# Kernel tuning notes

Measured on AMD Instinct MI355X. Metric: run time of the kernel, lower is better.

The kernel has to match this reference:

```python
import jax, jax.numpy as jnp
import numpy as np

N = 2048  # number of graph nodes


def setup_inputs() -> dict:
    key = jax.random.key(0)
    k1, k2, k3, k4 = jax.random.split(key, 4)
    # dense non-negative adjacency / association matrix
    A = jax.random.uniform(k1, (N, N), dtype=jnp.float32)
    # GTConv weights: layer0.conv1, layer0.conv2, layer1.conv1 (each (2,1,1,1))
    w1a = jax.random.normal(k2, (2, 1, 1, 1), dtype=jnp.float32)
    w1b = jax.random.normal(k3, (2, 1, 1, 1), dtype=jnp.float32)
    w2a = jax.random.normal(k4, (2, 1, 1, 1), dtype=jnp.float32)
    return {"A": A, "w1a": w1a, "w1b": w1b, "w2a": w2a}


def _gtconv(A4, w):
    # A4: (1,1,n,n); w: (2,1,1,1). softmax over dim=1 (singleton -> ones),
    # broadcast-multiply -> (2,1,n,n), sum over dim 0 -> (1,n,n)
    sw = jax.nn.softmax(w, axis=1)
    return jnp.sum(A4 * sw, axis=0)


def _norm(H):
    # H: (n,n). H <- diag(deg)^-1 @ (H + I), expressed as a row-scale
    # (identical math to the diagonal mm in the original).
    n = H.shape[0]
    H = H + jnp.eye(n, dtype=H.dtype)
    deg = jnp.sum(H, axis=1)
    deg = jnp.where(deg <= 1e-10, jnp.ones_like(deg), deg)
    return H / deg[:, None]


def reference(A, w1a, w1b, w2a):
    A4 = A[None, None]  # (1,1,n,n) after the forward's unsqueeze + broadcast
    # layer 0 (first=True)
    a = _gtconv(A4, w1a)            # (1,n,n)
    b = _gtconv(A4, w1b)            # (1,n,n)
    H = jnp.matmul(a, b)            # (1,n,n)
    # layer 1 (first=False): normalization of H[0], then bmm with conv(A)
    H_ = _norm(H[0])[None]          # (1,n,n)
    a2 = _gtconv(A4, w2a)           # (1,n,n)
    H2 = jnp.matmul(H_, a2)         # (1,n,n)
    return H2
```

## Files before the change

### kernel.cpp

```cpp
#include <hip/hip_runtime.h>
#include <stdint.h>

#define N 2048
#define TILE 128
#define BK 64
#define KH 16
#define RSTR 16
#define NN ((size_t)N * (size_t)N)

typedef unsigned short u16;
typedef __bf16 bf16x8 __attribute__((ext_vector_type(8)));
typedef unsigned short ushortx8 __attribute__((ext_vector_type(8)));
typedef float floatx4 __attribute__((ext_vector_type(4)));

static __device__ __forceinline__ u16 f2bf(float f) {
  unsigned int u = __builtin_bit_cast(unsigned int, f);
  return (u16)((u + 0x7fffu + ((u >> 16) & 1u)) >> 16);
}
static __device__ __forceinline__ float bf2f(u16 h) {
  unsigned int u = ((unsigned int)h) << 16;
  return __builtin_bit_cast(float, u);
}

static __device__ __forceinline__ void gload16(const u16* g, u16* l) {
  __builtin_amdgcn_global_load_lds(
      (const __attribute__((address_space(1))) void*)g,
      (__attribute__((address_space(3))) void*)l, 16, 0, 0);
}

__global__ void cast_tr(const float* __restrict__ A, u16* __restrict__ Ab,
                        u16* __restrict__ Abt) {
  __shared__ float tile[32][33];
  const int tx = threadIdx.x, ty = threadIdx.y;
  const int c = blockIdx.x * 32 + tx;
#pragma unroll
  for (int i = 0; i < 4; i++) {
    const int r = blockIdx.y * 32 + ty + i * 8;
    const float v = A[(size_t)r * N + c];
    Ab[(size_t)r * N + c] = f2bf(v);
    tile[ty + i * 8][tx] = v;
  }
  __syncthreads();
  const int r2 = blockIdx.y * 32 + tx;
#pragma unroll
  for (int i = 0; i < 4; i++) {
    const int c2 = blockIdx.x * 32 + ty + i * 8;
    Abt[(size_t)c2 * N + r2] = f2bf(tile[tx][ty + i * 8]);
  }
}

__device__ __forceinline__ void gemm_core(const u16* __restrict__ L,
                                          const u16* __restrict__ Rt,
                                          int row0, int col0,
                                          float res[4][4]) {
  __shared__ __align__(16) u16 As[2][2][TILE * BK];
  __shared__ __align__(16) u16 Bs[2][2][TILE * BK];

  const int t = threadIdx.x;
  const int lane = t & 63;
  const int w = t >> 6;
  const int h = w >> 3;
  const int wv = w & 7;

  const int rl = lane >> 3;
  const int cl = ((lane & 7) ^ rl) * 8;
  const int g0 = wv * 2;
  const u16* gA0 = L + (size_t)(row0 + g0 * 8 + rl) * N + h * (KH * BK) + cl;
  const u16* gA1 = gA0 + 8 * N;
  const u16* gB0 = Rt + (size_t)(col0 + g0 * 8 + rl) * N + h * (KH * BK) + cl;
  const u16* gB1 = gB0 + 8 * N;
  const int ld0 = g0 * 512;

  const int sub = wv;
  const int wr = (sub >> 2) * 64;
  const int wc = (sub & 3) * 32;
  const int lr = lane & 15;
  const int q = lane >> 4;
  const int lx = lr & 7;
  const int arow = (wr + lr) * BK;
  const int brow = (wc + lr) * BK;

  floatx4 acc[4][2];
#pragma unroll
  for (int i = 0; i < 4; i++)
#pragma unroll
    for (int j = 0; j < 2; j++) acc[i][j] = (floatx4){0.f, 0.f, 0.f, 0.f};

  gload16(gA0, &As[h][0][ld0]);
  gload16(gA1, &As[h][0][ld0 + 512]);
  gload16(gB0, &Bs[h][0][ld0]);
  gload16(gB1, &Bs[h][0][ld0 + 512]);
  __syncthreads();

#define GSTEP(i, cur, nxt)                                                    \
  {                                                                           \
    if ((i) + 1 < KH) {                                                       \
      gload16(gA0 + ((i) + 1) * BK, &As[h][nxt][ld0]);                        \
      gload16(gA1 + ((i) + 1) * BK, &As[h][nxt][ld0 + 512]);                  \
      gload16(gB0 + ((i) + 1) * BK, &Bs[h][nxt][ld0]);                        \
      gload16(gB1 + ((i) + 1) * BK, &Bs[h][nxt][ld0 + 512]);                  \
    }                                                                         \
    _Pragma("unroll") for (int kk = 0; kk < 2; kk++) {                        \
      bf16x8 af[4], bfr[2];                                                   \
      _Pragma("unroll") for (int mt = 0; mt < 4; mt++) af[mt] =               \
          __builtin_bit_cast(                                                 \
              bf16x8, *(const ushortx8*)&As[h][cur][arow + mt * 16 * BK +     \
                                                    ((kk * 4 + q) ^ lx) * 8]); \
      _Pragma("unroll") for (int nt = 0; nt < 2; nt++) bfr[nt] =              \
          __builtin_bit_cast(                                                 \
              bf16x8, *(const ushortx8*)&Bs[h][cur][brow + nt * 16 * BK +     \
                                                    ((kk * 4 + q) ^ lx) * 8]); \
      _Pragma("unroll") for (int mt = 0; mt < 4; mt++)                        \
          _Pragma("unroll") for (int nt = 0; nt < 2; nt++) acc[mt][nt] =      \
              __builtin_amdgcn_mfma_f32_16x16x32_bf16(af[mt], bfr[nt],        \
                                                      acc[mt][nt], 0, 0, 0);  \
    }                                                                         \
    __syncthreads();                                                          \
  }

  for (int io = 0; io < KH; io += 2) {
    GSTEP(io, 0, 1)
    GSTEP(io + 1, 1, 0)
  }
#undef GSTEP

  float* red = (float*)&As[0][0][0];
  const int oh = 1 - h;
  const int rship = (sub * 2 + oh) * (64 * RSTR);
  const int rkeep = (sub * 2 + h) * (64 * RSTR);
#pragma unroll
  for (int mt = 0; mt < 4; mt++)
#pragma unroll
    for (int r = 0; r < 4; r++) {
      const float vship = h ? acc[mt][0][r] : acc[mt][1][r];
      red[rship + (mt * 16 + q * 4 + r) * RSTR + lr] = vship;
    }
  __syncthreads();
#pragma unroll
  for (int mt = 0; mt < 4; mt++)
#pragma unroll
    for (int r = 0; r < 4; r++) {
      const float vkeep = h ? acc[mt][1][r] : acc[mt][0][r];
      res[mt][r] = vkeep + red[rkeep + (mt * 16 + q * 4 + r) * RSTR + lr];
    }
}

__global__ __launch_bounds__(1024, 4) void gemm_aa(const u16* __restrict__ Ab,
                                                   const u16* __restrict__ Abt,
                                                   u16* __restrict__ Mb) {
  const int row0 = blockIdx.y * TILE, col0 = blockIdx.x * TILE;
  float res[4][4];
  gemm_core(Ab, Abt, row0, col0, res);
  const int t = threadIdx.x;
  const int lane = t & 63, w = t >> 6;
  const int sub = w & 7, h = w >> 3;
  const int wr = (sub >> 2) * 64, wc = (sub & 3) * 32;
  const int lr = lane & 15, q = lane >> 4;
  const int cc = col0 + wc + h * 16 + lr;
#pragma unroll
  for (int mt = 0; mt < 4; mt++)
#pragma unroll
    for (int r = 0; r < 4; r++) {
      const int rr = row0 + wr + mt * 16 + q * 4 + r;
      Mb[(size_t)rr * N + cc] = f2bf(res[mt][r]);
    }
}

__global__ void rowsum_k(const u16* __restrict__ Mb, float* __restrict__ rdeg) {
  const int row = blockIdx.x;
  const int t = threadIdx.x;
  const ushortx8 v = *((const ushortx8*)(Mb + (size_t)row * N) + t);
  float s = 0.f;
#pragma unroll
  for (int j = 0; j < 8; j++) s += bf2f(v[j]);
#pragma unroll
  for (int off = 32; off > 0; off >>= 1) s += __shfl_down(s, off, 64);
  __shared__ float ws[4];
  if ((t & 63) == 0) ws[t >> 6] = s;
  __syncthreads();
  if (t == 0) {
    float d = 4.f * (ws[0] + ws[1] + ws[2] + ws[3]) + 1.f;
    if (d <= 1e-10f) d = 1.f;
    rdeg[row] = 1.f / d;
  }
}

__global__ __launch_bounds__(1024, 4) void gemm_ma(const u16* __restrict__ Mb,
                                                   const u16* __restrict__ Abt,
                                                   const float* __restrict__ A,
                                                   const float* __restrict__ rdeg,
                                                   float* __restrict__ out) {
  const int row0 = blockIdx.y * TILE, col0 = blockIdx.x * TILE;
  float res[4][4];
  gemm_core(Mb, Abt, row0, col0, res);
  const int t = threadIdx.x;
  const int lane = t & 63, w = t >> 6;
  const int sub = w & 7, h = w >> 3;
  const int wr = (sub >> 2) * 64, wc = (sub & 3) * 32;
  const int lr = lane & 15, q = lane >> 4;
  const int cc = col0 + wc + h * 16 + lr;
#pragma unroll
  for (int mt = 0; mt < 4; mt++)
#pragma unroll
    for (int r = 0; r < 4; r++) {
      const int rr = row0 + wr + mt * 16 + q * 4 + r;
      out[(size_t)rr * N + cc] =
          (8.f * res[mt][r] + 2.f * A[(size_t)rr * N + cc]) * rdeg[rr];
    }
}

extern "C" void kernel_launch(void* const* d_in, const int* in_sizes, int n_in,
                              void* d_out, int out_size, void* d_ws, size_t ws_size,
                              hipStream_t stream) {
  const float* A = (const float*)d_in[0];
  float* out = (float*)d_out;
  char* ws = (char*)d_ws;
  u16* Ab = (u16*)ws;
  u16* Abt = (u16*)(ws + NN * 2);
  u16* Mb = (u16*)(ws + NN * 4);
  float* rdeg = (float*)(ws + NN * 6);

  cast_tr<<<dim3(N / 32, N / 32), dim3(32, 8), 0, stream>>>(A, Ab, Abt);
  gemm_aa<<<dim3(N / TILE, N / TILE), 1024, 0, stream>>>(Ab, Abt, Mb);
  rowsum_k<<<N, 256, 0, stream>>>(Mb, rdeg);
  gemm_ma<<<dim3(N / TILE, N / TILE), 1024, 0, stream>>>(Mb, Abt, A, rdeg, out);
}
```

Baseline: 135.2 us.

## Restructure GEMM core into 4-way split-K with 64x64 warp tiles

Reorganizes the shared GEMM core so the 16 waves form four K-slices of four waves each. Each wave now computes a 64x64 sub-tile, up from 64x32, which raises MFMA work per LDS fragment load. The async global-to-LDS loads are replaced by register-staged loads written into padded LDS rows, with BK halved. A two-stage LDS reduction merges the four K partials and only half the waves write outputs. The cost is higher register pressure, extra reduction syncs, and software-pipelined register staging in place of direct LDS loads.

```diff
diff --git a/kernel.cpp b/kernel.cpp
--- a/kernel.cpp
+++ b/kernel.cpp
@@ -3,9 +3,10 @@
 
 #define N 2048
 #define TILE 128
-#define BK 64
-#define KH 16
-#define RSTR 16
+#define BK 32
+#define KQ 16
+#define LDSW 40
+#define XSTR 68
 #define NN ((size_t)N * (size_t)N)
 
 typedef unsigned short u16;
@@ -20,12 +21,6 @@
 static __device__ __forceinline__ float bf2f(u16 h) {
   unsigned int u = ((unsigned int)h) << 16;
   return __builtin_bit_cast(float, u);
-}
-
-static __device__ __forceinline__ void gload16(const u16* g, u16* l) {
-  __builtin_amdgcn_global_load_lds(
-      (const __attribute__((address_space(1))) void*)g,
-      (__attribute__((address_space(3))) void*)l, 16, 0, 0);
 }
 
 __global__ void cast_tr(const float* __restrict__ A, u16* __restrict__ Ab,
@@ -52,117 +47,167 @@
 __device__ __forceinline__ void gemm_core(const u16* __restrict__ L,
                                           const u16* __restrict__ Rt,
                                           int row0, int col0,
-                                          float res[4][4]) {
-  __shared__ __align__(16) u16 As[2][2][TILE * BK];
-  __shared__ __align__(16) u16 Bs[2][2][TILE * BK];
+                                          float res[4][8]) {
+  __shared__ __align__(16) u16 AB[2][4][2][TILE * LDSW];
+  static_assert(sizeof(u16) * 2 * 4 * 2 * TILE * LDSW == 163840, "LDS size");
 
   const int t = threadIdx.x;
   const int lane = t & 63;
   const int w = t >> 6;
-  const int h = w >> 3;
-  const int wv = w & 7;
-
-  const int rl = lane >> 3;
-  const int cl = ((lane & 7) ^ rl) * 8;
-  const int g0 = wv * 2;
-  const u16* gA0 = L + (size_t)(row0 + g0 * 8 + rl) * N + h * (KH * BK) + cl;
-  const u16* gA1 = gA0 + 8 * N;
-  const u16* gB0 = Rt + (size_t)(col0 + g0 * 8 + rl) * N + h * (KH * BK) + cl;
-  const u16* gB1 = gB0 + 8 * N;
-  const int ld0 = g0 * 512;
-
-  const int sub = wv;
-  const int wr = (sub >> 2) * 64;
-  const int wc = (sub & 3) * 32;
+  const int k = w >> 2;
+  const int p = w & 3;
+  const int tl = t & 255;
+
+  const int srow = tl >> 2;
+  const int sch = (tl & 3) * 8;
+  const u16* gA0 = L + (size_t)(row0 + srow) * N + k * (KQ * BK) + sch;
+  const u16* gA1 = gA0 + (size_t)64 * N;
+  const u16* gB0 = Rt + (size_t)(col0 + srow) * N + k * (KQ * BK) + sch;
+  const u16* gB1 = gB0 + (size_t)64 * N;
+  const int w0 = srow * LDSW + sch;
+  const int w1 = w0 + 64 * LDSW;
+
   const int lr = lane & 15;
   const int q = lane >> 4;
-  const int lx = lr & 7;
-  const int arow = (wr + lr) * BK;
-  const int brow = (wc + lr) * BK;
-
-  floatx4 acc[4][2];
+  const int wr = (p >> 1) * 64;
+  const int wc = (p & 1) * 64;
+  const int abase = (wr + lr) * LDSW + q * 8;
+  const int bbase = (wc + lr) * LDSW + q * 8;
+
+  floatx4 acc[4][4];
 #pragma unroll
   for (int i = 0; i < 4; i++)
 #pragma unroll
-    for (int j = 0; j < 2; j++) acc[i][j] = (floatx4){0.f, 0.f, 0.f, 0.f};
-
-  gload16(gA0, &As[h][0][ld0]);
-  gload16(gA1, &As[h][0][ld0 + 512]);
-  gload16(gB0, &Bs[h][0][ld0]);
-  gload16(gB1, &Bs[h][0][ld0 + 512]);
+    for (int j = 0; j < 4; j++) acc[i][j] = (floatx4){0.f, 0.f, 0.f, 0.f};
+
+  {
+    const ushortx8 pa0 = *(const ushortx8*)gA0;
+    const ushortx8 pa1 = *(const ushortx8*)gA1;
+    const ushortx8 pb0 = *(const ushortx8*)gB0;
+    const ushortx8 pb1 = *(const ushortx8*)gB1;
+    *(ushortx8*)&AB[0][k][0][w0] = pa0;
+    *(ushortx8*)&AB[0][k][0][w1] = pa1;
+    *(ushortx8*)&AB[1][k][0][w0] = pb0;
+    *(ushortx8*)&AB[1][k][0][w1] = pb1;
+  }
   __syncthreads();
 
 #define GSTEP(i, cur, nxt)                                                    \
   {                                                                           \
-    if ((i) + 1 < KH) {                                                       \
-      gload16(gA0 + ((i) + 1) * BK, &As[h][nxt][ld0]);                        \
-      gload16(gA1 + ((i) + 1) * BK, &As[h][nxt][ld0 + 512]);                  \
-      gload16(gB0 + ((i) + 1) * BK, &Bs[h][nxt][ld0]);                        \
-      gload16(gB1 + ((i) + 1) * BK, &Bs[h][nxt][ld0 + 512]);                  \
+    ushortx8 pa0, pa1, pb0, pb1;                                              \
+    if ((i) + 1 < KQ) {                                                       \
+      pa0 = *(const ushortx8*)(gA0 + ((i) + 1) * BK);                         \
+      pa1 = *(const ushortx8*)(gA1 + ((i) + 1) * BK);                         \
+      pb0 = *(const ushortx8*)(gB0 + ((i) + 1) * BK);                         \
+      pb1 = *(const ushortx8*)(gB1 + ((i) + 1) * BK);                         \
     }                                                                         \
-    _Pragma("unroll") for (int kk = 0; kk < 2; kk++) {                        \
-      bf16x8 af[4], bfr[2];                                                   \
-      _Pragma("unroll") for (int mt = 0; mt < 4; mt++) af[mt] =               \
-          __builtin_bit_cast(                                                 \
-              bf16x8, *(const ushortx8*)&As[h][cur][arow + mt * 16 * BK +     \
-                                                    ((kk * 4 + q) ^ lx) * 8]); \
-      _Pragma("unroll") for (int nt = 0; nt < 2; nt++) bfr[nt] =              \
-          __builtin_bit_cast(                                                 \
-              bf16x8, *(const ushortx8*)&Bs[h][cur][brow + nt * 16 * BK +     \
-                                                    ((kk * 4 + q) ^ lx) * 8]); \
-      _Pragma("unroll") for (int mt = 0; mt < 4; mt++)                        \
-          _Pragma("unroll") for (int nt = 0; nt < 2; nt++) acc[mt][nt] =      \
-              __builtin_amdgcn_mfma_f32_16x16x32_bf16(af[mt], bfr[nt],        \
-                                                      acc[mt][nt], 0, 0, 0);  \
+    bf16x8 af[4], bfr[4];                                                     \
+    _Pragma("unroll") for (int mt = 0; mt < 4; mt++) af[mt] =                 \
+        __builtin_bit_cast(bf16x8,                                            \
+            *(const ushortx8*)&AB[0][k][cur][abase + mt * 16 * LDSW]);        \
+    _Pragma("unroll") for (int nt = 0; nt < 4; nt++) bfr[nt] =                \
+        __builtin_bit_cast(bf16x8,                                            \
+            *(const ushortx8*)&AB[1][k][cur][bbase + nt * 16 * LDSW]);        \
+    _Pragma("unroll") for (int mt = 0; mt < 4; mt++)                          \
+        _Pragma("unroll") for (int nt = 0; nt < 4; nt++) acc[mt][nt] =        \
+            __builtin_amdgcn_mfma_f32_16x16x32_bf16(af[mt], bfr[nt],          \
+                                                    acc[mt][nt], 0, 0, 0);    \
+    if ((i) + 1 < KQ) {                                                       \
+      *(ushortx8*)&AB[0][k][nxt][w0] = pa0;                                   \
+      *(ushortx8*)&AB[0][k][nxt][w1] = pa1;                                   \
+      *(ushortx8*)&AB[1][k][nxt][w0] = pb0;                                   \
+      *(ushortx8*)&AB[1][k][nxt][w1] = pb1;                                   \
     }                                                                         \
     __syncthreads();                                                          \
   }
 
-  for (int io = 0; io < KH; io += 2) {
+  for (int io = 0; io < KQ; io += 2) {
     GSTEP(io, 0, 1)
     GSTEP(io + 1, 1, 0)
   }
 #undef GSTEP
 
-  float* red = (float*)&As[0][0][0];
-  const int oh = 1 - h;
-  const int rship = (sub * 2 + oh) * (64 * RSTR);
-  const int rkeep = (sub * 2 + h) * (64 * RSTR);
-#pragma unroll
-  for (int mt = 0; mt < 4; mt++)
-#pragma unroll
-    for (int r = 0; r < 4; r++) {
-      const float vship = h ? acc[mt][0][r] : acc[mt][1][r];
-      red[rship + (mt * 16 + q * 4 + r) * RSTR + lr] = vship;
-    }
-  __syncthreads();
-#pragma unroll
-  for (int mt = 0; mt < 4; mt++)
-#pragma unroll
-    for (int r = 0; r < 4; r++) {
-      const float vkeep = h ? acc[mt][1][r] : acc[mt][0][r];
-      res[mt][r] = vkeep + red[rkeep + (mt * 16 + q * 4 + r) * RSTR + lr];
-    }
+  float* red = (float*)&AB[0][0][0][0];
+  const int slot1 = (p * 2 + (k >> 1)) * (64 * XSTR);
+  if (k & 1) {
+#pragma unroll
+    for (int mt = 0; mt < 4; mt++)
+#pragma unroll
+      for (int nt = 0; nt < 4; nt++)
+#pragma unroll
+        for (int r = 0; r < 4; r++)
+          red[slot1 + (mt * 16 + q * 4 + r) * XSTR + nt * 16 + lr] =
+              acc[mt][nt][r];
+  }
+  __syncthreads();
+  if (!(k & 1)) {
+#pragma unroll
+    for (int mt = 0; mt < 4; mt++)
+#pragma unroll
+      for (int nt = 0; nt < 4; nt++)
+#pragma unroll
+        for (int r = 0; r < 4; r++)
+          acc[mt][nt][r] +=
+              red[slot1 + (mt * 16 + q * 4 + r) * XSTR + nt * 16 + lr];
+  }
+  __syncthreads();
+  if (k == 0) {
+    const int s = (p * 2 + 1) * (64 * XSTR);
+#pragma unroll
+    for (int mt = 0; mt < 4; mt++)
+#pragma unroll
+      for (int j = 0; j < 2; j++)
+#pragma unroll
+        for (int r = 0; r < 4; r++)
+          red[s + (mt * 16 + q * 4 + r) * XSTR + j * 16 + lr] =
+              acc[mt][2 + j][r];
+  } else if (k == 2) {
+    const int s = (p * 2) * (64 * XSTR);
+#pragma unroll
+    for (int mt = 0; mt < 4; mt++)
+#pragma unroll
+      for (int j = 0; j < 2; j++)
+#pragma unroll
+        for (int r = 0; r < 4; r++)
+          red[s + (mt * 16 + q * 4 + r) * XSTR + j * 16 + lr] = acc[mt][j][r];
+  }
+  __syncthreads();
+  if (!(k & 1)) {
+    const int s = (k == 0 ? p * 2 : p * 2 + 1) * (64 * XSTR);
+#pragma unroll
+    for (int mt = 0; mt < 4; mt++)
+#pragma unroll
+      for (int j = 0; j < 2; j++)
+#pragma unroll
+        for (int r = 0; r < 4; r++) {
+          const float vkeep = (k == 0) ? acc[mt][j][r] : acc[mt][2 + j][r];
+          res[mt][j * 4 + r] =
+              vkeep + red[s + (mt * 16 + q * 4 + r) * XSTR + j * 16 + lr];
+        }
+  }
 }
 
 __global__ __launch_bounds__(1024, 4) void gemm_aa(const u16* __restrict__ Ab,
                                                    const u16* __restrict__ Abt,
                                                    u16* __restrict__ Mb) {
   const int row0 = blockIdx.y * TILE, col0 = blockIdx.x * TILE;
-  float res[4][4];
+  float res[4][8];
   gemm_core(Ab, Abt, row0, col0, res);
   const int t = threadIdx.x;
   const int lane = t & 63, w = t >> 6;
-  const int sub = w & 7, h = w >> 3;
-  const int wr = (sub >> 2) * 64, wc = (sub & 3) * 32;
+  const int k = w >> 2, p = w & 3;
+  if (k & 1) return;
+  const int wr = (p >> 1) * 64, wc = (p & 1) * 64;
   const int lr = lane & 15, q = lane >> 4;
-  const int cc = col0 + wc + h * 16 + lr;
+  const int cbase = col0 + wc + (k == 2 ? 32 : 0);
 #pragma unroll
   for (int mt = 0; mt < 4; mt++)
 #pragma unroll
     for (int r = 0; r < 4; r++) {
       const int rr = row0 + wr + mt * 16 + q * 4 + r;
-      Mb[(size_t)rr * N + cc] = f2bf(res[mt][r]);
+#pragma unroll
+      for (int j = 0; j < 2; j++)
+        Mb[(size_t)rr * N + cbase + j * 16 + lr] = f2bf(res[mt][j * 4 + r]);
     }
 }
 
@@ -191,21 +236,27 @@
                                                    const float* __restrict__ rdeg,
                                                    float* __restrict__ out) {
   const int row0 = blockIdx.y * TILE, col0 = blockIdx.x * TILE;
-  float res[4][4];
+  float res[4][8];
   gemm_core(Mb, Abt, row0, col0, res);
   const int t = threadIdx.x;
   const int lane = t & 63, w = t >> 6;
-  const int sub = w & 7, h = w >> 3;
-  const int wr = (sub >> 2) * 64, wc = (sub & 3) * 32;
+  const int k = w >> 2, p = w & 3;
+  if (k & 1) return;
+  const int wr = (p >> 1) * 64, wc = (p & 1) * 64;
   const int lr = lane & 15, q = lane >> 4;
-  const int cc = col0 + wc + h * 16 + lr;
+  const int cbase = col0 + wc + (k == 2 ? 32 : 0);
 #pragma unroll
   for (int mt = 0; mt < 4; mt++)
 #pragma unroll
     for (int r = 0; r < 4; r++) {
       const int rr = row0 + wr + mt * 16 + q * 4 + r;
-      out[(size_t)rr * N + cc] =
-          (8.f * res[mt][r] + 2.f * A[(size_t)rr * N + cc]) * rdeg[rr];
+      const float rd = rdeg[rr];
+#pragma unroll
+      for (int j = 0; j < 2; j++) {
+        const int cc = cbase + j * 16 + lr;
+        out[(size_t)rr * N + cc] =
+            (8.f * res[mt][j * 4 + r] + 2.f * A[(size_t)rr * N + cc]) * rd;
+      }
     }
 }
 
```

After: 140.7 us. +4.0%, slower.

## Shrink GEMM tiles to 128x64 with register-staged loads and padded LDS

Applied to the files above, without the earlier changes.

Both GEMM kernels now use 128x64 tiles with 512-thread blocks and a K-step of 32, which doubles the block count so the grid fills more of the GPU. The direct global-to-LDS loads are replaced by register prefetch two steps ahead, with stores into padded LDS rows instead of XOR swizzling. The split-K reduction stride is padded to avoid bank conflicts. In exchange, each block reuses less data, performs more barriers per unit of work, and holds extra registers for the staged loads.

```diff
diff --git a/kernel.cpp b/kernel.cpp
--- a/kernel.cpp
+++ b/kernel.cpp
@@ -2,10 +2,12 @@
 #include <stdint.h>
 
 #define N 2048
-#define TILE 128
-#define BK 64
-#define KH 16
-#define RSTR 16
+#define TM 128
+#define TN 64
+#define BK 32
+#define KH 32
+#define LDSW 40
+#define RSTR 17
 #define NN ((size_t)N * (size_t)N)
 
 typedef unsigned short u16;
@@ -20,12 +22,6 @@
 static __device__ __forceinline__ float bf2f(u16 h) {
   unsigned int u = ((unsigned int)h) << 16;
   return __builtin_bit_cast(float, u);
-}
-
-static __device__ __forceinline__ void gload16(const u16* g, u16* l) {
-  __builtin_amdgcn_global_load_lds(
-      (const __attribute__((address_space(1))) void*)g,
-      (__attribute__((address_space(3))) void*)l, 16, 0, 0);
 }
 
 __global__ void cast_tr(const float* __restrict__ A, u16* __restrict__ Ab,
@@ -53,32 +49,31 @@
                                           const u16* __restrict__ Rt,
                                           int row0, int col0,
                                           float res[4][4]) {
-  __shared__ __align__(16) u16 As[2][2][TILE * BK];
-  __shared__ __align__(16) u16 Bs[2][2][TILE * BK];
+  __shared__ __align__(16) u16 As[2][2][TM * LDSW];
+  __shared__ __align__(16) u16 Bs[2][2][TN * LDSW];
 
   const int t = threadIdx.x;
   const int lane = t & 63;
   const int w = t >> 6;
-  const int h = w >> 3;
-  const int wv = w & 7;
-
-  const int rl = lane >> 3;
-  const int cl = ((lane & 7) ^ rl) * 8;
-  const int g0 = wv * 2;
-  const u16* gA0 = L + (size_t)(row0 + g0 * 8 + rl) * N + h * (KH * BK) + cl;
-  const u16* gA1 = gA0 + 8 * N;
-  const u16* gB0 = Rt + (size_t)(col0 + g0 * 8 + rl) * N + h * (KH * BK) + cl;
-  const u16* gB1 = gB0 + 8 * N;
-  const int ld0 = g0 * 512;
-
-  const int sub = wv;
-  const int wr = (sub >> 2) * 64;
-  const int wc = (sub & 3) * 32;
+  const int h = w >> 2;
+  const int sub = w & 3;
+  const int tl = t & 255;
+
+  const int srow = tl >> 2;
+  const int sch = (tl & 3) * 8;
+  const u16* gA0 = L + (size_t)(row0 + srow) * N + h * (KH * BK) + sch;
+  const u16* gA1 = gA0 + (size_t)64 * N;
+  const u16* gB0 = Rt + (size_t)(col0 + srow) * N + h * (KH * BK) + sch;
+  const int wA0 = srow * LDSW + sch;
+  const int wA1 = wA0 + 64 * LDSW;
+  const int wB0 = wA0;
+
   const int lr = lane & 15;
   const int q = lane >> 4;
-  const int lx = lr & 7;
-  const int arow = (wr + lr) * BK;
-  const int brow = (wc + lr) * BK;
+  const int wr = (sub >> 1) * 64;
+  const int wc = (sub & 1) * 32;
+  const int abase = (wr + lr) * LDSW + q * 8;
+  const int bbase = (wc + lr) * LDSW + q * 8;
 
   floatx4 acc[4][2];
 #pragma unroll
@@ -86,34 +81,40 @@
 #pragma unroll
     for (int j = 0; j < 2; j++) acc[i][j] = (floatx4){0.f, 0.f, 0.f, 0.f};
 
-  gload16(gA0, &As[h][0][ld0]);
-  gload16(gA1, &As[h][0][ld0 + 512]);
-  gload16(gB0, &Bs[h][0][ld0]);
-  gload16(gB1, &Bs[h][0][ld0 + 512]);
+  ushortx8 sA0[2], sA1[2], sB[2];
+  sA0[0] = *(const ushortx8*)(gA0);
+  sA1[0] = *(const ushortx8*)(gA1);
+  sB[0] = *(const ushortx8*)(gB0);
+  sA0[1] = *(const ushortx8*)(gA0 + BK);
+  sA1[1] = *(const ushortx8*)(gA1 + BK);
+  sB[1] = *(const ushortx8*)(gB0 + BK);
+  *(ushortx8*)&As[h][0][wA0] = sA0[0];
+  *(ushortx8*)&As[h][0][wA1] = sA1[0];
+  *(ushortx8*)&Bs[h][0][wB0] = sB[0];
   __syncthreads();
 
 #define GSTEP(i, cur, nxt)                                                    \
   {                                                                           \
+    if ((i) + 2 < KH) {                                                       \
+      sA0[cur] = *(const ushortx8*)(gA0 + ((i) + 2) * BK);                    \
+      sA1[cur] = *(const ushortx8*)(gA1 + ((i) + 2) * BK);                    \
+      sB[cur] = *(const ushortx8*)(gB0 + ((i) + 2) * BK);                     \
+    }                                                                         \
+    bf16x8 af[4], bfr[2];                                                     \
+    _Pragma("unroll") for (int mt = 0; mt < 4; mt++) af[mt] =                 \
+        __builtin_bit_cast(bf16x8,                                            \
+            *(const ushortx8*)&As[h][cur][abase + mt * 16 * LDSW]);           \
+    _Pragma("unroll") for (int nt = 0; nt < 2; nt++) bfr[nt] =                \
+        __builtin_bit_cast(bf16x8,                                            \
+            *(const ushortx8*)&Bs[h][cur][bbase + nt * 16 * LDSW]);           \
+    _Pragma("unroll") for (int mt = 0; mt < 4; mt++)                          \
+        _Pragma("unroll") for (int nt = 0; nt < 2; nt++) acc[mt][nt] =        \
+            __builtin_amdgcn_mfma_f32_16x16x32_bf16(af[mt], bfr[nt],          \
+                                                    acc[mt][nt], 0, 0, 0);    \
     if ((i) + 1 < KH) {                                                       \
-      gload16(gA0 + ((i) + 1) * BK, &As[h][nxt][ld0]);                        \
-      gload16(gA1 + ((i) + 1) * BK, &As[h][nxt][ld0 + 512]);                  \
-      gload16(gB0 + ((i) + 1) * BK, &Bs[h][nxt][ld0]);                        \
-      gload16(gB1 + ((i) + 1) * BK, &Bs[h][nxt][ld0 + 512]);                  \
-    }                                                                         \
-    _Pragma("unroll") for (int kk = 0; kk < 2; kk++) {                        \
-      bf16x8 af[4], bfr[2];                                                   \
-      _Pragma("unroll") for (int mt = 0; mt < 4; mt++) af[mt] =               \
-          __builtin_bit_cast(                                                 \
-              bf16x8, *(const ushortx8*)&As[h][cur][arow + mt * 16 * BK +     \
-                                                    ((kk * 4 + q) ^ lx) * 8]); \
-      _Pragma("unroll") for (int nt = 0; nt < 2; nt++) bfr[nt] =              \
-          __builtin_bit_cast(                                                 \
-              bf16x8, *(const ushortx8*)&Bs[h][cur][brow + nt * 16 * BK +     \
-                                                    ((kk * 4 + q) ^ lx) * 8]); \
-      _Pragma("unroll") for (int mt = 0; mt < 4; mt++)                        \
-          _Pragma("unroll") for (int nt = 0; nt < 2; nt++) acc[mt][nt] =      \
-              __builtin_amdgcn_mfma_f32_16x16x32_bf16(af[mt], bfr[nt],        \
-                                                      acc[mt][nt], 0, 0, 0);  \
+      *(ushortx8*)&As[h][nxt][wA0] = sA0[nxt];                                \
+      *(ushortx8*)&As[h][nxt][wA1] = sA1[nxt];                                \
+      *(ushortx8*)&Bs[h][nxt][wB0] = sB[nxt];                                 \
     }                                                                         \
     __syncthreads();                                                          \
   }
@@ -145,16 +146,16 @@
     }
 }
 
-__global__ __launch_bounds__(1024, 4) void gemm_aa(const u16* __restrict__ Ab,
-                                                   const u16* __restrict__ Abt,
-                                                   u16* __restrict__ Mb) {
-  const int row0 = blockIdx.y * TILE, col0 = blockIdx.x * TILE;
+__global__ __launch_bounds__(512, 4) void gemm_aa(const u16* __restrict__ Ab,
+                                                  const u16* __restrict__ Abt,
+                                                  u16* __restrict__ Mb) {
+  const int row0 = blockIdx.y * TM, col0 = blockIdx.x * TN;
   float res[4][4];
   gemm_core(Ab, Abt, row0, col0, res);
   const int t = threadIdx.x;
   const int lane = t & 63, w = t >> 6;
-  const int sub = w & 7, h = w >> 3;
-  const int wr = (sub >> 2) * 64, wc = (sub & 3) * 32;
+  const int sub = w & 3, h = w >> 2;
+  const int wr = (sub >> 1) * 64, wc = (sub & 1) * 32;
   const int lr = lane & 15, q = lane >> 4;
   const int cc = col0 + wc + h * 16 + lr;
 #pragma unroll
@@ -185,18 +186,18 @@
   }
 }
 
-__global__ __launch_bounds__(1024, 4) void gemm_ma(const u16* __restrict__ Mb,
-                                                   const u16* __restrict__ Abt,
-                                                   const float* __restrict__ A,
-                                                   const float* __restrict__ rdeg,
-                                                   float* __restrict__ out) {
-  const int row0 = blockIdx.y * TILE, col0 = blockIdx.x * TILE;
+__global__ __launch_bounds__(512, 4) void gemm_ma(const u16* __restrict__ Mb,
+                                                  const u16* __restrict__ Abt,
+                                                  const float* __restrict__ A,
+                                                  const float* __restrict__ rdeg,
+                                                  float* __restrict__ out) {
+  const int row0 = blockIdx.y * TM, col0 = blockIdx.x * TN;
   float res[4][4];
   gemm_core(Mb, Abt, row0, col0, res);
   const int t = threadIdx.x;
   const int lane = t & 63, w = t >> 6;
-  const int sub = w & 7, h = w >> 3;
-  const int wr = (sub >> 2) * 64, wc = (sub & 3) * 32;
+  const int sub = w & 3, h = w >> 2;
+  const int wr = (sub >> 1) * 64, wc = (sub & 1) * 32;
   const int lr = lane & 15, q = lane >> 4;
   const int cc = col0 + wc + h * 16 + lr;
 #pragma unroll
@@ -221,7 +222,7 @@
   float* rdeg = (float*)(ws + NN * 6);
 
   cast_tr<<<dim3(N / 32, N / 32), dim3(32, 8), 0, stream>>>(A, Ab, Abt);
-  gemm_aa<<<dim3(N / TILE, N / TILE), 1024, 0, stream>>>(Ab, Abt, Mb);
+  gemm_aa<<<dim3(N / TN, N / TM), 512, 0, stream>>>(Ab, Abt, Mb);
   rowsum_k<<<N, 256, 0, stream>>>(Mb, rdeg);
-  gemm_ma<<<dim3(N / TILE, N / TILE), 1024, 0, stream>>>(Mb, Abt, A, rdeg, out);
-}
+  gemm_ma<<<dim3(N / TN, N / TM), 512, 0, stream>>>(Mb, Abt, A, rdeg, out);
+}
```

New measurement: 141.3 us. 1.05x slower.
